# Performance work log

Hardware: AMD Instinct MI355X
Metric: run time of the kernel (lower is better)

## Reference

```python
import jax, jax.numpy as jnp
import numpy as np

# dims
N, E, Z, C, NB = 8192, 131072, 10, 128, 8
R_MAX, P_CUT, AVG_NEIGH = 5.0, 5, 16.0
SH_DIM, N_L, N_LAYERS, MLP_H = 16, 4, 2, 16
# which l each of the 16 sh components belongs to
L_OF_M = jnp.array([0, 1, 1, 1, 2, 2, 2, 2, 2, 3, 3, 3, 3, 3, 3, 3])


def spherical_harmonics(u):
    """Real spherical harmonics up to l=3, e3nn 'component' normalization. u: [E,3] unit vectors."""
    x, y, z = u[:, 0], u[:, 1], u[:, 2]
    x2, y2, z2 = x * x, y * y, z * z
    s3, s5, s15 = np.sqrt(3.0), np.sqrt(5.0), np.sqrt(15.0)
    a33, a32, a31, a30 = 0.25 * np.sqrt(70.0), np.sqrt(105.0), 0.25 * np.sqrt(42.0), 0.5 * np.sqrt(7.0)
    Y = [jnp.ones_like(x),
         s3 * x, s3 * y, s3 * z,
         s15 * x * y, s15 * y * z, 0.5 * s5 * (3 * z2 - 1.0), s15 * x * z, 0.5 * s15 * (x2 - y2),
         a33 * y * (3 * x2 - y2), a32 * x * y * z, a31 * y * (5 * z2 - 1.0),
         a30 * z * (5 * z2 - 3.0), a31 * x * (5 * z2 - 1.0), 0.5 * a32 * z * (x2 - y2),
         a33 * x * (x2 - 3 * y2)]
    return jnp.stack(Y, axis=-1)  # [E,16]


def radial_embedding(r):
    """Bessel radial basis with smooth polynomial cutoff (p=5). r: [E] edge lengths."""
    x = r / R_MAX
    p = float(P_CUT)
    cut = (1.0 - 0.5 * (p + 1.0) * (p + 2.0) * x ** P_CUT
           + p * (p + 2.0) * x ** (P_CUT + 1) - 0.5 * p * (p + 1.0) * x ** (P_CUT + 2))
    cut = jnp.where(x < 1.0, cut, 0.0)
    n = jnp.arange(1, NB + 1, dtype=r.dtype)
    bessel = np.sqrt(2.0 / R_MAX) * jnp.sin(n[None, :] * jnp.pi * x[:, None]) / r[:, None]
    return bessel * cut[:, None]  # [E,8]


def _forward(positions, node_attrs, shifts, W_embed, W_up, R_w1, R_w2, R_w3,
             W_out, w_sc, w_prod, W_plin, w_ro0, ro_w1, ro_w2, edge_index):
    sender, receiver = edge_index[0], edge_index[1]
    vec = positions[receiver] - positions[sender] + shifts          # [E,3]
    lengths = jnp.linalg.norm(vec, axis=-1) + 1e-9                  # [E]
    sh = spherical_harmonics(vec / lengths[:, None])                # [E,16]
    edge_feats = radial_embedding(lengths)                          # [E,8]

    # node embedding: scalars into l=0 slot of [N,C,16]
    scalars = node_attrs @ W_embed                                  # [N,C]
    feats = jnp.zeros((N, C, SH_DIM), scalars.dtype).at[:, :, 0].set(scalars)

    outputs = []
    for L in range(N_LAYERS):
        # linear up (channel mixing, per irrep component)
        h = jnp.einsum('ncm,cd->ndm', feats, W_up[L])               # [N,C,16]
        # radial MLP -> per-edge, per-channel, per-l tensor-product weights
        r = jax.nn.silu(edge_feats @ R_w1[L])
        r = jax.nn.silu(r @ R_w2[L])
        w = (r @ R_w3[L]).reshape(E, C, N_L)                        # [E,C,4]
        w_m = jnp.take(w, L_OF_M, axis=2)                           # [E,C,16]
        # channel-wise tensor product: scalar node feat x SH, scatter to receiver
        msg = h[sender, :, 0][:, :, None] * w_m * sh[:, None, :]    # [E,C,16]
        agg = jax.ops.segment_sum(msg, receiver, num_segments=N) / AVG_NEIGH
        m = jnp.einsum('ncm,cd->ndm', agg, W_out[L])                # [N,C,16]
        # element-dependent skip connection
        sc = h * (node_attrs @ w_sc[L])[:, :, None]
        # product basis (correlation 3): element-weighted powers of scalar part
        s = m[:, :, 0]                                              # [N,C]
        coeff = jnp.einsum('nz,zck->nck', node_attrs, w_prod[L])    # [N,C,3]
        powers = jnp.stack([jnp.ones_like(s), s, s * s], axis=-1)   # [N,C,3]
        scale = jnp.sum(coeff * powers, axis=-1)                    # [N,C]
        feats = jnp.einsum('ncm,cd->ndm', m * scale[:, :, None], W_plin[L]) + sc
        if L == 0:
            outputs.append(feats[:, :, 0] @ w_ro0)                  # linear readout [N]
        else:
            outputs.append(jax.nn.silu(feats[:, :, 0] @ ro_w1) @ ro_w2)  # nonlinear readout [N]
    return outputs[0] + outputs[1]


def setup_inputs() -> dict:
    key = jax.random.key(0)
    ks = jax.random.split(key, 16)
    positions = jax.random.normal(ks[0], (N, 3), jnp.float32) * 1.5
    elems = jax.random.randint(ks[1], (N,), 0, Z)
    node_attrs = jax.nn.one_hot(elems, Z, dtype=jnp.float32)
    edge_index = jax.random.randint(ks[2], (2, E), 0, N)
    shifts = jnp.zeros((E, 3), jnp.float32)
    g = lambda k, sh, fan: jax.random.normal(k, sh, jnp.float32) / np.sqrt(fan)
    return {
        'positions': positions, 'node_attrs': node_attrs, 'shifts': shifts,
        'W_embed': g(ks[3], (Z, C), Z),
        'W_up': g(ks[4], (N_LAYERS, C, C), C),
        'R_w1': g(ks[5], (N_LAYERS, NB, 64), NB),
        'R_w2': g(ks[6], (N_LAYERS, 64, 64), 64),
        'R_w3': g(ks[7], (N_LAYERS, 64, C * N_L), 64),
        'W_out': g(ks[8], (N_LAYERS, C, C), C),
        'w_sc': g(ks[9], (N_LAYERS, Z, C), 1),
        'w_prod': g(ks[10], (N_LAYERS, Z, C, 3), 1) * 0.1,
        'W_plin': g(ks[11], (N_LAYERS, C, C), C),
        'w_ro0': g(ks[12], (C,), C),
        'ro_w1': g(ks[13], (C, MLP_H), C),
        'ro_w2': g(ks[14], (MLP_H,), MLP_H),
        'edge_index': edge_index,
    }


def reference(positions, node_attrs, shifts, W_embed, W_up, R_w1, R_w2, R_w3,
              W_out, w_sc, w_prod, W_plin, w_ro0, ro_w1, ro_w2, edge_index):
    return _forward(positions, node_attrs, shifts, W_embed, W_up, R_w1, R_w2, R_w3,
                    W_out, w_sc, w_prod, W_plin, w_ro0, ro_w1, ro_w2, edge_index)
```

## Files before the change

kernel.cpp:

```cpp
#include <hip/hip_runtime.h>
#include <math.h>

constexpr int kN = 8192;
constexpr int kE = 131072;
constexpr int NPB = 16;

typedef short bf16x8 __attribute__((ext_vector_type(8)));
typedef float f32x4 __attribute__((ext_vector_type(4)));
typedef unsigned short ushort_t;
typedef unsigned int uint_t;

__device__ __forceinline__ float silu_f(float x) { return x / (1.f + __expf(-x)); }

__device__ __forceinline__ ushort_t f2b(float f) {
  uint_t x = __float_as_uint(f);
  uint_t r = (x + 0x7fffu + ((x >> 16) & 1u)) >> 16;
  return (ushort_t)r;
}
__device__ __forceinline__ float b2f(ushort_t u) {
  return __uint_as_float(((uint_t)u) << 16);
}

__global__ __launch_bounds__(256) void zero_ints_kernel(int* __restrict__ a, int* __restrict__ b) {
  int i = blockIdx.x * 256 + threadIdx.x;
  if (i < kN) { a[i] = 0; b[i] = 0; }
}

__global__ __launch_bounds__(256) void elem_kernel(const float* __restrict__ attrs, int* __restrict__ elem) {
  int n = blockIdx.x * 256 + threadIdx.x;
  if (n >= kN) return;
  const float* a = attrs + (size_t)n * 10;
  int best = 0; float bv = a[0];
  #pragma unroll
  for (int z = 1; z < 10; ++z) { float v = a[z]; if (v > bv) { bv = v; best = z; } }
  elem[n] = best;
}

__global__ __launch_bounds__(256) void init_feats_kernel(const float* __restrict__ W_embed,
                                                         const int* __restrict__ elem,
                                                         ushort_t* __restrict__ F) {
  int i = blockIdx.x * 256 + threadIdx.x;
  int n = i >> 7, c = i & 127;
  F[(size_t)n * 2048 + c] = f2b(W_embed[(size_t)elem[n] * 128 + c]);
}

__global__ __launch_bounds__(256) void count_kernel(const int* __restrict__ ei, int* __restrict__ counts) {
  int e = blockIdx.x * 256 + threadIdx.x;
  if (e < kE) atomicAdd(&counts[ei[kE + e]], 1);
}

__global__ __launch_bounds__(1024) void scan_kernel(const int* __restrict__ counts, int* __restrict__ offs) {
  __shared__ int tmp[1024];
  int t = threadIdx.x;
  int loc[8]; int s = 0;
  #pragma unroll
  for (int i = 0; i < 8; ++i) { loc[i] = s; s += counts[t*8 + i]; }
  tmp[t] = s;
  __syncthreads();
  for (int d = 1; d < 1024; d <<= 1) {
    int v = (t >= d) ? tmp[t - d] : 0;
    __syncthreads();
    tmp[t] += v;
    __syncthreads();
  }
  int pre = (t == 0) ? 0 : tmp[t - 1];
  #pragma unroll
  for (int i = 0; i < 8; ++i) offs[t*8 + i] = pre + loc[i];
  if (t == 1023) offs[kN] = tmp[1023];
}

__global__ __launch_bounds__(256) void fill_kernel(const int* __restrict__ ei, const int* __restrict__ offs,
                                                   int* __restrict__ cursor, int* __restrict__ eids,
                                                   int* __restrict__ sends) {
  int e = blockIdx.x * 256 + threadIdx.x;
  if (e >= kE) return;
  int s = ei[e];
  int r = ei[kE + e];
  int pos = atomicAdd(&cursor[r], 1);
  eids[offs[r] + pos] = e;
  sends[offs[r] + pos] = s;
}

__global__ __launch_bounds__(256) void geom_kernel(const float* __restrict__ pos,
                                                   const float* __restrict__ shifts,
                                                   const int* __restrict__ ei,
                                                   const int* __restrict__ eids,
                                                   const int* __restrict__ sends,
                                                   float* __restrict__ sh,
                                                   float* __restrict__ rb) {
  int slot = blockIdx.x * 256 + threadIdx.x;
  if (slot >= kE) return;
  int e = eids[slot];
  int s = sends[slot];
  int r = ei[kE + e];
  float vx = pos[r*3+0] - pos[s*3+0] + shifts[(size_t)e*3+0];
  float vy = pos[r*3+1] - pos[s*3+1] + shifts[(size_t)e*3+1];
  float vz = pos[r*3+2] - pos[s*3+2] + shifts[(size_t)e*3+2];
  float len = sqrtf(vx*vx + vy*vy + vz*vz) + 1e-9f;
  float inv = 1.f / len;
  float x = vx*inv, y = vy*inv, z = vz*inv;
  float x2 = x*x, y2 = y*y, z2 = z*z;
  const float s3  = 1.7320508075688772f;
  const float s5  = 2.2360679774997896f;
  const float s15 = 3.8729833462074170f;
  const float a33 = 2.0916500663351889f;
  const float a32 = 10.246950765959598f;
  const float a31 = 1.6201851746019651f;
  const float a30 = 1.3228756555322954f;
  float4* shp = (float4*)(sh + (size_t)slot * 16);
  shp[0] = make_float4(1.f, s3*x, s3*y, s3*z);
  shp[1] = make_float4(s15*x*y, s15*y*z, 0.5f*s5*(3.f*z2 - 1.f), s15*x*z);
  shp[2] = make_float4(0.5f*s15*(x2 - y2), a33*y*(3.f*x2 - y2), a32*x*y*z, a31*y*(5.f*z2 - 1.f));
  shp[3] = make_float4(a30*z*(5.f*z2 - 3.f), a31*x*(5.f*z2 - 1.f), 0.5f*a32*z*(x2 - y2), a33*x*(x2 - 3.f*y2));
  float xr = len * 0.2f;
  float cut = 0.f;
  if (xr < 1.f) {
    float x5 = xr*xr*xr*xr*xr;
    cut = 1.f - 21.f*x5 + 35.f*x5*xr - 15.f*x5*xr*xr;
  }
  float pref = 0.63245553203367587f * cut * inv;
  const float PI = 3.14159265358979323846f;
  float theta = PI * xr;
  float sn, cs;
  __sincosf(theta, &sn, &cs);
  float twoc = 2.f * cs;
  float b[8];
  float s_prev = 0.f, s_cur = sn;
  b[0] = pref * s_cur;
  #pragma unroll
  for (int k = 1; k < 8; ++k) {
    float s_next = twoc * s_cur - s_prev;
    s_prev = s_cur; s_cur = s_next;
    b[k] = pref * s_cur;
  }
  float4* rbp = (float4*)(rb + (size_t)slot * 8);
  rbp[0] = make_float4(b[0], b[1], b[2], b[3]);
  rbp[1] = make_float4(b[4], b[5], b[6], b[7]);
}

__global__ __launch_bounds__(256) void radial_kernel(const float* __restrict__ rb,
                                                     const float* __restrict__ W1,
                                                     const float* __restrict__ W2,
                                                     ushort_t* __restrict__ r2) {
  __shared__ float rbs[128][8];
  __shared__ float W1s[8*64];
  __shared__ ushort_t B2s[64][72];
  __shared__ ushort_t r1s[128][72];
  const int tid = threadIdx.x;
  const size_t ebase = (size_t)blockIdx.x * 128;
  {
    int r = tid >> 1, q = tid & 1;
    *(float4*)&rbs[r][q*4] = *(const float4*)&rb[(ebase + r)*8 + q*4];
  }
  for (int i = tid; i < 512; i += 256) W1s[i] = W1[i];
  for (int i = tid; i < 4096; i += 256) {
    int k = i >> 6, col = i & 63;
    B2s[col][k] = f2b(W2[i]);
  }
  __syncthreads();
  {
    int col = tid & 63;
    int r0 = (tid >> 6) * 32;
    #pragma unroll 4
    for (int rr = 0; rr < 32; ++rr) {
      int row = r0 + rr;
      float v = 0.f;
      #pragma unroll
      for (int i = 0; i < 8; ++i) v = fmaf(rbs[row][i], W1s[i*64 + col], v);
      r1s[row][col] = f2b(silu_f(v));
    }
  }
  __syncthreads();
  const int lane = tid & 63, wv = tid >> 6;
  const int wr = wv * 32;
  const int fr = lane & 15, kg = (lane >> 4) * 8;
  f32x4 acc[2][4] = {};
  #pragma unroll
  for (int ks = 0; ks < 2; ++ks) {
    const int k0 = ks*32 + kg;
    bf16x8 af[2], bfr[4];
    #pragma unroll
    for (int i = 0; i < 2; ++i) af[i] = *(const bf16x8*)&r1s[wr + i*16 + fr][k0];
    #pragma unroll
    for (int j = 0; j < 4; ++j) bfr[j] = *(const bf16x8*)&B2s[j*16 + fr][k0];
    #pragma unroll
    for (int i = 0; i < 2; ++i)
      #pragma unroll
      for (int j = 0; j < 4; ++j)
        acc[i][j] = __builtin_amdgcn_mfma_f32_16x16x32_bf16(af[i], bfr[j], acc[i][j], 0, 0, 0);
  }
  __syncthreads();
  const int dcol = lane & 15, drow4 = (lane >> 4) * 4;
  #pragma unroll
  for (int i = 0; i < 2; ++i)
    #pragma unroll
    for (int j = 0; j < 4; ++j)
      #pragma unroll
      for (int r = 0; r < 4; ++r) {
        int row = wr + i*16 + drow4 + r;
        int col = j*16 + dcol;
        r1s[row][col] = f2b(silu_f(acc[i][j][r]));
      }
  __syncthreads();
  for (int idx = tid * 8; idx < 128*64; idx += 256*8) {
    int r = idx >> 6, k = idx & 63;
    *(int4*)&r2[(ebase + r)*64 + k] = *(const int4*)&r1s[r][k];
  }
}

__global__ __launch_bounds__(256) void transpose_w_kernel(const float* __restrict__ W, ushort_t* __restrict__ WT) {
  int i = blockIdx.x * 256 + threadIdx.x;
  int d = i >> 7, c = i & 127;
  WT[i] = f2b(W[c*128 + d]);
}

__global__ __launch_bounds__(256) void transpose_r3_kernel(const float* __restrict__ R3, ushort_t* __restrict__ R3T) {
  int i = blockIdx.x * 256 + threadIdx.x;
  int t = i >> 6, j = i & 63;
  int c = t & 127, l = t >> 7;
  R3T[i] = f2b(R3[j*512 + c*4 + l]);
}

template<bool SCALED, bool EPI, bool L0>
__global__ __launch_bounds__(256) void mgemm_kernel(
    const ushort_t* __restrict__ A, size_t aStride,
    const ushort_t* __restrict__ BT,
    ushort_t* __restrict__ O, size_t oStride,
    const float* __restrict__ scaleBuf,
    const ushort_t* __restrict__ Hbuf,
    const float* __restrict__ wscL,
    const int* __restrict__ elem)
{
  __shared__ ushort_t As[128][136];
  __shared__ ushort_t Bs[128][136];
  const int tid = threadIdx.x;
  const size_t rowbase = (size_t)blockIdx.x * 128;

  for (int idx = tid * 8; idx < 128 * 128; idx += 256 * 8) {
    int r = idx >> 7, k = idx & 127;
    *(int4*)&Bs[r][k] = *(const int4*)&BT[(size_t)r * 128 + k];
  }
  for (int idx = tid * 8; idx < 128 * 128; idx += 256 * 8) {
    int r = idx >> 7, k = idx & 127;
    size_t grow = rowbase + r;
    const ushort_t* ap = A + grow * aStride + k;
    if (SCALED) {
      const float* sp = scaleBuf + (grow >> 4) * 128 + k;
      uint_t u[4];
      #pragma unroll
      for (int q = 0; q < 4; ++q) {
        ushort_t lo = f2b(b2f(ap[2*q])   * sp[2*q]);
        ushort_t hi = f2b(b2f(ap[2*q+1]) * sp[2*q+1]);
        u[q] = (uint_t)lo | ((uint_t)hi << 16);
      }
      *(int4*)&As[r][k] = make_int4((int)u[0], (int)u[1], (int)u[2], (int)u[3]);
    } else {
      *(int4*)&As[r][k] = *(const int4*)ap;
    }
  }
  __syncthreads();

  const int lane = tid & 63, wv = tid >> 6;
  const int wr = (wv >> 1) * 64, wc = (wv & 1) * 64;
  const int fr = lane & 15;
  const int kg = (lane >> 4) * 8;
  f32x4 acc[4][4] = {};
  #pragma unroll
  for (int ks = 0; ks < 4; ++ks) {
    const int k0 = ks * 32 + kg;
    bf16x8 af[4], bfr[4];
    #pragma unroll
    for (int i = 0; i < 4; ++i) af[i]  = *(const bf16x8*)&As[wr + i*16 + fr][k0];
    #pragma unroll
    for (int j = 0; j < 4; ++j) bfr[j] = *(const bf16x8*)&Bs[wc + j*16 + fr][k0];
    #pragma unroll
    for (int i = 0; i < 4; ++i)
      #pragma unroll
      for (int j = 0; j < 4; ++j)
        acc[i][j] = __builtin_amdgcn_mfma_f32_16x16x32_bf16(af[i], bfr[j], acc[i][j], 0, 0, 0);
  }

  const int dcol = lane & 15, drow4 = (lane >> 4) * 4;
  #pragma unroll
  for (int i = 0; i < 4; ++i) {
    #pragma unroll
    for (int j = 0; j < 4; ++j) {
      int col = wc + j*16 + dcol;
      #pragma unroll
      for (int r = 0; r < 4; ++r) {
        int row = wr + i*16 + drow4 + r;
        size_t grow = rowbase + row;
        float v = acc[i][j][r];
        if (EPI) {
          if (!L0 || ((grow & 15) == 0)) {
            int ee = elem[grow >> 4];
            v += b2f(Hbuf[grow * 128 + col]) * wscL[(size_t)ee * 128 + col];
          }
        }
        O[grow * oStride + col] = f2b(v);
      }
    }
  }
}

__global__ __launch_bounds__(512, 1) void gather_kernel(
    const int* __restrict__ offs, const int* __restrict__ sends,
    const ushort_t* __restrict__ r2csr,
    const float* __restrict__ shcsr,
    const ushort_t* __restrict__ R3T,
    const ushort_t* __restrict__ H,
    ushort_t* __restrict__ AGG)
{
  __shared__ ushort_t R3Ts[512][68];
  __shared__ ushort_t r2s[2][32][68];
  __shared__ ushort_t h0s[2][32][132];
  __shared__ float    shs[2][32][16];
  const int tid = threadIdx.x;
  const int lane = tid & 63, wid = tid >> 6;
  const int l = wid >> 1, cb = (wid & 1) * 64;
  const int mb = l * l, mc = 2 * l + 1;
  const int fr = lane & 15, kg = (lane >> 4) * 8;
  const int n0 = blockIdx.x * NPB;
  const int hslot = tid >> 4, hseg = tid & 15;
  const int rslot = tid >> 3, rseg = tid & 7;
  const int xs = tid - 256, sslot = xs >> 2, sseg = xs & 3;

  for (int idx = tid; idx < 4096; idx += 512) {
    int tr = idx >> 3, seg = idx & 7;
    *(int4*)&R3Ts[tr][seg * 8] = *(const int4*)&R3T[(size_t)tr * 64 + seg * 8];
  }
  {
    int a0 = offs[n0], a1 = offs[n0 + 1];
    int4 h0v = make_int4(0,0,0,0), r2v = make_int4(0,0,0,0);
    float4 shv = make_float4(0.f,0.f,0.f,0.f);
    if (a0 + hslot < a1) h0v = *(const int4*)&H[(size_t)sends[a0 + hslot] * 2048 + hseg * 8];
    if (tid < 256 && a0 + rslot < a1) r2v = *(const int4*)&r2csr[(size_t)(a0 + rslot) * 64 + rseg * 8];
    if (tid >= 256 && tid < 384 && a0 + sslot < a1) shv = *(const float4*)&shcsr[(size_t)(a0 + sslot) * 16 + sseg * 4];
    *(int4*)&h0s[0][hslot][hseg * 8] = h0v;
    if (tid < 256) *(int4*)&r2s[0][rslot][rseg * 8] = r2v;
    else if (tid < 384) *(float4*)&shs[0][sslot][sseg * 4] = shv;
  }
  __syncthreads();

  int p = 0;
  for (int nn = n0; nn < n0 + NPB; ++nn) {
    const int e0n = offs[nn], e1n = offs[nn + 1];
    int4 h0n = make_int4(0,0,0,0), r2n = make_int4(0,0,0,0);
    float4 shn = make_float4(0.f,0.f,0.f,0.f);
    if (nn + 1 < n0 + NPB) {
      int a0 = offs[nn + 1], a1 = offs[nn + 2];
      if (a0 + hslot < a1) h0n = *(const int4*)&H[(size_t)sends[a0 + hslot] * 2048 + hseg * 8];
      if (tid < 256 && a0 + rslot < a1) r2n = *(const int4*)&r2csr[(size_t)(a0 + rslot) * 64 + rseg * 8];
      if (tid >= 256 && tid < 384 && a0 + sslot < a1) shn = *(const float4*)&shcsr[(size_t)(a0 + sslot) * 16 + sseg * 4];
    }

    float agg[7][4] = {};
    auto compute = [&](int pb) {
      f32x4 acc[2][4] = {};
      #pragma unroll
      for (int ks = 0; ks < 2; ++ks) {
        bf16x8 af[2], bfr[4];
        #pragma unroll
        for (int i = 0; i < 2; ++i) af[i] = *(const bf16x8*)&r2s[pb][i*16 + fr][ks*32 + kg];
        #pragma unroll
        for (int j = 0; j < 4; ++j) bfr[j] = *(const bf16x8*)&R3Ts[wid*64 + j*16 + fr][ks*32 + kg];
        #pragma unroll
        for (int i = 0; i < 2; ++i)
          #pragma unroll
          for (int j = 0; j < 4; ++j)
            acc[i][j] = __builtin_amdgcn_mfma_f32_16x16x32_bf16(af[i], bfr[j], acc[i][j], 0, 0, 0);
      }
      #pragma unroll
      for (int i = 0; i < 2; ++i)
        #pragma unroll
        for (int r = 0; r < 4; ++r) {
          int slot = i*16 + ((lane >> 4) << 2) + r;
          float shr[7];
          #pragma unroll
          for (int mi = 0; mi < 7; ++mi) shr[mi] = shs[pb][slot][mb + mi];
          #pragma unroll
          for (int j = 0; j < 4; ++j) {
            float wh = acc[i][j][r] * b2f(h0s[pb][slot][cb + j*16 + fr]);
            #pragma unroll
            for (int mi = 0; mi < 7; ++mi)
              if (mi < mc) agg[mi][j] = fmaf(wh, shr[mi], agg[mi][j]);
          }
        }
    };
    compute(p);
    for (int base = e0n + 32; base < e1n; base += 32) {
      __syncthreads();
      int4 h0x = make_int4(0,0,0,0), r2x = make_int4(0,0,0,0);
      float4 shx = make_float4(0.f,0.f,0.f,0.f);
      if (base + hslot < e1n) h0x = *(const int4*)&H[(size_t)sends[base + hslot] * 2048 + hseg * 8];
      if (tid < 256 && base + rslot < e1n) r2x = *(const int4*)&r2csr[(size_t)(base + rslot) * 64 + rseg * 8];
      if (tid >= 256 && tid < 384 && base + sslot < e1n) shx = *(const float4*)&shcsr[(size_t)(base + sslot) * 16 + sseg * 4];
      *(int4*)&h0s[p][hslot][hseg * 8] = h0x;
      if (tid < 256) *(int4*)&r2s[p][rslot][rseg * 8] = r2x;
      else if (tid < 384) *(float4*)&shs[p][sslot][sseg * 4] = shx;
      __syncthreads();
      compute(p);
    }
    #pragma unroll
    for (int mi = 0; mi < 7; ++mi) {
      if (mi < mc) {
        #pragma unroll
        for (int j = 0; j < 4; ++j) {
          float v = agg[mi][j];
          v += __shfl_xor(v, 16, 64);
          v += __shfl_xor(v, 32, 64);
          if (lane < 16)
            AGG[(size_t)nn * 2048 + (mb + mi) * 128 + cb + j * 16 + lane] = f2b(v * 0.0625f);
        }
      }
    }
    *(int4*)&h0s[p ^ 1][hslot][hseg * 8] = h0n;
    if (tid < 256) *(int4*)&r2s[p ^ 1][rslot][rseg * 8] = r2n;
    else if (tid < 384) *(float4*)&shs[p ^ 1][sslot][sseg * 4] = shn;
    __syncthreads();
    p ^= 1;
  }
}

__global__ __launch_bounds__(256) void scale_kernel(const ushort_t* __restrict__ M,
                                                    const int* __restrict__ elem,
                                                    const float* __restrict__ wprodL,
                                                    float* __restrict__ scale) {
  int i = blockIdx.x * 256 + threadIdx.x;
  int n = i >> 7, c = i & 127;
  float s = b2f(M[(size_t)n * 2048 + c]);
  const float* co = wprodL + ((size_t)elem[n] * 128 + c) * 3;
  scale[i] = co[0] + s * (co[1] + s * co[2]);
}

__global__ __launch_bounds__(64) void readout_kernel(const ushort_t* __restrict__ F,
                                                     const float* __restrict__ ro0,
                                                     const float* __restrict__ ro1,
                                                     const float* __restrict__ ro2,
                                                     float* __restrict__ out, int layer) {
  int n = blockIdx.x; int t = threadIdx.x;
  const ushort_t* fr = F + (size_t)n * 2048;
  float f0 = b2f(fr[t]), f1 = b2f(fr[t + 64]);
  if (layer == 0) {
    float v = f0 * ro0[t] + f1 * ro0[t + 64];
    #pragma unroll
    for (int m = 32; m > 0; m >>= 1) v += __shfl_xor(v, m, 64);
    if (t == 0) out[n] = v;
  } else {
    float acc = 0.f;
    for (int h = 0; h < 16; ++h) {
      float p = f0 * ro1[t*16 + h] + f1 * ro1[(t + 64)*16 + h];
      #pragma unroll
      for (int m = 32; m > 0; m >>= 1) p += __shfl_xor(p, m, 64);
      acc = fmaf(silu_f(p), ro2[h], acc);
    }
    if (t == 0) out[n] += acc;
  }
}

extern "C" void kernel_launch(void* const* d_in, const int* in_sizes, int n_in,
                              void* d_out, int out_size, void* d_ws, size_t ws_size,
                              hipStream_t stream) {
  (void)in_sizes; (void)n_in; (void)out_size;
  const float* positions = (const float*)d_in[0];
  const float* node_attrs= (const float*)d_in[1];
  const float* shifts    = (const float*)d_in[2];
  const float* W_embed   = (const float*)d_in[3];
  const float* W_up      = (const float*)d_in[4];
  const float* R_w1      = (const float*)d_in[5];
  const float* R_w2      = (const float*)d_in[6];
  const float* R_w3      = (const float*)d_in[7];
  const float* W_out     = (const float*)d_in[8];
  const float* w_sc      = (const float*)d_in[9];
  const float* w_prod    = (const float*)d_in[10];
  const float* W_plin    = (const float*)d_in[11];
  const float* w_ro0     = (const float*)d_in[12];
  const float* ro_w1     = (const float*)d_in[13];
  const float* ro_w2     = (const float*)d_in[14];
  const int*   ei        = (const int*)d_in[15];
  float* out = (float*)d_out;

  char* ws_ptr = (char*)d_ws;
  size_t off = 0;
  auto alloc = [&](size_t nbytes) -> void* {
    void* p = ws_ptr + off;
    off += (nbytes + 255) & ~(size_t)255;
    return p;
  };
  const size_t PB = (size_t)kN * 16 * 128 * sizeof(ushort_t);
  ushort_t* P0    = (ushort_t*)alloc(PB);
  ushort_t* P1    = (ushort_t*)alloc(PB);
  ushort_t* P2    = (ushort_t*)alloc(PB);
  float* shcsr    = (float*)alloc((size_t)kE * 16 * 4);
  float* rbcsr    = (float*)alloc((size_t)kE * 8 * 4);
  ushort_t* r2csr = (ushort_t*)alloc((size_t)kE * 64 * 2);
  float* scaleb   = (float*)alloc((size_t)kN * 128 * 4);
  ushort_t* R3T0  = (ushort_t*)alloc(512 * 64 * 2);
  ushort_t* R3T1  = (ushort_t*)alloc(512 * 64 * 2);
  ushort_t* WTu0  = (ushort_t*)alloc(128 * 128 * 2);
  ushort_t* WTu1  = (ushort_t*)alloc(128 * 128 * 2);
  ushort_t* WTo0  = (ushort_t*)alloc(128 * 128 * 2);
  ushort_t* WTo1  = (ushort_t*)alloc(128 * 128 * 2);
  ushort_t* WTp0  = (ushort_t*)alloc(128 * 128 * 2);
  ushort_t* WTp1  = (ushort_t*)alloc(128 * 128 * 2);
  int* elemb  = (int*)alloc(kN * 4);
  int* counts = (int*)alloc(kN * 4);
  int* cursor = (int*)alloc(kN * 4);
  int* offsb  = (int*)alloc((kN + 1) * 4);
  int* eidsb  = (int*)alloc((size_t)kE * 4);
  int* sendsb = (int*)alloc((size_t)kE * 4);
  if (off > ws_size) return;

  zero_ints_kernel<<<kN/256, 256, 0, stream>>>(counts, cursor);
  elem_kernel<<<kN/256, 256, 0, stream>>>(node_attrs, elemb);
  init_feats_kernel<<<(kN*128)/256, 256, 0, stream>>>(W_embed, elemb, P0);
  count_kernel<<<kE/256, 256, 0, stream>>>(ei, counts);
  scan_kernel<<<1, 1024, 0, stream>>>(counts, offsb);
  fill_kernel<<<kE/256, 256, 0, stream>>>(ei, offsb, cursor, eidsb, sendsb);
  geom_kernel<<<kE/256, 256, 0, stream>>>(positions, shifts, ei, eidsb, sendsb, shcsr, rbcsr);
  transpose_w_kernel<<<64, 256, 0, stream>>>(W_up, WTu0);
  transpose_w_kernel<<<64, 256, 0, stream>>>(W_up + 16384, WTu1);
  transpose_w_kernel<<<64, 256, 0, stream>>>(W_out, WTo0);
  transpose_w_kernel<<<64, 256, 0, stream>>>(W_out + 16384, WTo1);
  transpose_w_kernel<<<64, 256, 0, stream>>>(W_plin, WTp0);
  transpose_w_kernel<<<64, 256, 0, stream>>>(W_plin + 16384, WTp1);
  transpose_r3_kernel<<<128, 256, 0, stream>>>(R_w3, R3T0);
  transpose_r3_kernel<<<128, 256, 0, stream>>>(R_w3 + 32768, R3T1);

  radial_kernel<<<kE/128, 256, 0, stream>>>(rbcsr, R_w1, R_w2, r2csr);
  mgemm_kernel<false,false,false><<<kN/128, 256, 0, stream>>>(
      P0, 2048, WTu0, P1, 2048, nullptr, nullptr, nullptr, nullptr);
  gather_kernel<<<kN/NPB, 512, 0, stream>>>(offsb, sendsb, r2csr, shcsr, R3T0, P1, P2);
  mgemm_kernel<false,false,false><<<(kN*16)/128, 256, 0, stream>>>(
      P2, 128, WTo0, P0, 128, nullptr, nullptr, nullptr, nullptr);
  scale_kernel<<<(kN*128)/256, 256, 0, stream>>>(P0, elemb, w_prod, scaleb);
  mgemm_kernel<true,true,true><<<(kN*16)/128, 256, 0, stream>>>(
      P0, 128, WTp0, P2, 128, scaleb, P1, w_sc, elemb);
  readout_kernel<<<kN, 64, 0, stream>>>(P2, w_ro0, ro_w1, ro_w2, out, 0);

  radial_kernel<<<kE/128, 256, 0, stream>>>(rbcsr, R_w1 + 512, R_w2 + 4096, r2csr);
  mgemm_kernel<false,false,false><<<(kN*16)/128, 256, 0, stream>>>(
      P2, 128, WTu1, P1, 128, nullptr, nullptr, nullptr, nullptr);
  gather_kernel<<<kN/NPB, 512, 0, stream>>>(offsb, sendsb, r2csr, shcsr, R3T1, P1, P0);
  mgemm_kernel<false,false,false><<<(kN*16)/128, 256, 0, stream>>>(
      P0, 128, WTo1, P2, 128, nullptr, nullptr, nullptr, nullptr);
  scale_kernel<<<(kN*128)/256, 256, 0, stream>>>(P2, elemb, w_prod + 3840, scaleb);
  mgemm_kernel<true,true,false><<<(kN*16)/128, 256, 0, stream>>>(
      P2, 128, WTp1, P0, 128, scaleb, P1, w_sc + 1280, elemb);
  readout_kernel<<<kN, 64, 0, stream>>>(P0, w_ro0, ro_w1, ro_w2, out, 1);
}
```

Before: 546.3 us.

## Split gather kernel channel halves across grid y with smaller blocks

```diff
diff --git a/kernel.cpp b/kernel.cpp
--- a/kernel.cpp
+++ b/kernel.cpp
@@ -303,7 +303,7 @@
   }
 }
 
-__global__ __launch_bounds__(512, 1) void gather_kernel(
+__global__ __launch_bounds__(256, 2) void gather_kernel(
     const int* __restrict__ offs, const int* __restrict__ sends,
     const ushort_t* __restrict__ r2csr,
     const float* __restrict__ shcsr,
@@ -311,34 +311,39 @@
     const ushort_t* __restrict__ H,
     ushort_t* __restrict__ AGG)
 {
-  __shared__ ushort_t R3Ts[512][68];
+  __shared__ ushort_t R3Ts[256][68];
   __shared__ ushort_t r2s[2][32][68];
-  __shared__ ushort_t h0s[2][32][132];
-  __shared__ float    shs[2][32][16];
+  __shared__ ushort_t h0s[2][32][68];
+  __shared__ float    shs[2][32][17];
   const int tid = threadIdx.x;
-  const int lane = tid & 63, wid = tid >> 6;
-  const int l = wid >> 1, cb = (wid & 1) * 64;
+  const int lane = tid & 63;
+  const int l = tid >> 6;
+  const int cbb = blockIdx.y * 64;
   const int mb = l * l, mc = 2 * l + 1;
-  const int fr = lane & 15, kg = (lane >> 4) * 8;
+  const int fr = lane & 15, g = lane >> 4, kg = g * 8;
   const int n0 = blockIdx.x * NPB;
-  const int hslot = tid >> 4, hseg = tid & 15;
-  const int rslot = tid >> 3, rseg = tid & 7;
-  const int xs = tid - 256, sslot = xs >> 2, sseg = xs & 3;
-
-  for (int idx = tid; idx < 4096; idx += 512) {
-    int tr = idx >> 3, seg = idx & 7;
-    *(int4*)&R3Ts[tr][seg * 8] = *(const int4*)&R3T[(size_t)tr * 64 + seg * 8];
+  const int hslot = tid >> 3, hseg = tid & 7;
+  const int s0i = tid, s1i = 256 + tid;
+
+  for (int idx = tid; idx < 2048; idx += 256) {
+    int lt = idx >> 3, seg = idx & 7;
+    int gt = (lt >> 6) * 128 + cbb + (lt & 63);
+    *(int4*)&R3Ts[lt][seg * 8] = *(const int4*)&R3T[(size_t)gt * 64 + seg * 8];
   }
   {
     int a0 = offs[n0], a1 = offs[n0 + 1];
     int4 h0v = make_int4(0,0,0,0), r2v = make_int4(0,0,0,0);
-    float4 shv = make_float4(0.f,0.f,0.f,0.f);
-    if (a0 + hslot < a1) h0v = *(const int4*)&H[(size_t)sends[a0 + hslot] * 2048 + hseg * 8];
-    if (tid < 256 && a0 + rslot < a1) r2v = *(const int4*)&r2csr[(size_t)(a0 + rslot) * 64 + rseg * 8];
-    if (tid >= 256 && tid < 384 && a0 + sslot < a1) shv = *(const float4*)&shcsr[(size_t)(a0 + sslot) * 16 + sseg * 4];
+    float sv0 = 0.f, sv1 = 0.f;
+    if (a0 + hslot < a1) {
+      h0v = *(const int4*)&H[(size_t)sends[a0 + hslot] * 2048 + cbb + hseg * 8];
+      r2v = *(const int4*)&r2csr[(size_t)(a0 + hslot) * 64 + hseg * 8];
+    }
+    if (a0 + (s0i >> 4) < a1) sv0 = shcsr[(size_t)(a0 + (s0i >> 4)) * 16 + (s0i & 15)];
+    if (a0 + (s1i >> 4) < a1) sv1 = shcsr[(size_t)(a0 + (s1i >> 4)) * 16 + (s1i & 15)];
     *(int4*)&h0s[0][hslot][hseg * 8] = h0v;
-    if (tid < 256) *(int4*)&r2s[0][rslot][rseg * 8] = r2v;
-    else if (tid < 384) *(float4*)&shs[0][sslot][sseg * 4] = shv;
+    *(int4*)&r2s[0][hslot][hseg * 8] = r2v;
+    shs[0][s0i >> 4][s0i & 15] = sv0;
+    shs[0][s1i >> 4][s1i & 15] = sv1;
   }
   __syncthreads();
 
@@ -346,12 +351,15 @@
   for (int nn = n0; nn < n0 + NPB; ++nn) {
     const int e0n = offs[nn], e1n = offs[nn + 1];
     int4 h0n = make_int4(0,0,0,0), r2n = make_int4(0,0,0,0);
-    float4 shn = make_float4(0.f,0.f,0.f,0.f);
+    float sn0 = 0.f, sn1 = 0.f;
     if (nn + 1 < n0 + NPB) {
       int a0 = offs[nn + 1], a1 = offs[nn + 2];
-      if (a0 + hslot < a1) h0n = *(const int4*)&H[(size_t)sends[a0 + hslot] * 2048 + hseg * 8];
-      if (tid < 256 && a0 + rslot < a1) r2n = *(const int4*)&r2csr[(size_t)(a0 + rslot) * 64 + rseg * 8];
-      if (tid >= 256 && tid < 384 && a0 + sslot < a1) shn = *(const float4*)&shcsr[(size_t)(a0 + sslot) * 16 + sseg * 4];
+      if (a0 + hslot < a1) {
+        h0n = *(const int4*)&H[(size_t)sends[a0 + hslot] * 2048 + cbb + hseg * 8];
+        r2n = *(const int4*)&r2csr[(size_t)(a0 + hslot) * 64 + hseg * 8];
+      }
+      if (a0 + (s0i >> 4) < a1) sn0 = shcsr[(size_t)(a0 + (s0i >> 4)) * 16 + (s0i & 15)];
+      if (a0 + (s1i >> 4) < a1) sn1 = shcsr[(size_t)(a0 + (s1i >> 4)) * 16 + (s1i & 15)];
     }
 
     float agg[7][4] = {};
@@ -363,7 +371,7 @@
         #pragma unroll
         for (int i = 0; i < 2; ++i) af[i] = *(const bf16x8*)&r2s[pb][i*16 + fr][ks*32 + kg];
         #pragma unroll
-        for (int j = 0; j < 4; ++j) bfr[j] = *(const bf16x8*)&R3Ts[wid*64 + j*16 + fr][ks*32 + kg];
+        for (int j = 0; j < 4; ++j) bfr[j] = *(const bf16x8*)&R3Ts[l*64 + j*16 + fr][ks*32 + kg];
         #pragma unroll
         for (int i = 0; i < 2; ++i)
           #pragma unroll
@@ -374,13 +382,13 @@
       for (int i = 0; i < 2; ++i)
         #pragma unroll
         for (int r = 0; r < 4; ++r) {
-          int slot = i*16 + ((lane >> 4) << 2) + r;
+          int slot = i*16 + g*4 + r;
           float shr[7];
           #pragma unroll
           for (int mi = 0; mi < 7; ++mi) shr[mi] = shs[pb][slot][mb + mi];
           #pragma unroll
           for (int j = 0; j < 4; ++j) {
-            float wh = acc[i][j][r] * b2f(h0s[pb][slot][cb + j*16 + fr]);
+            float wh = acc[i][j][r] * b2f(h0s[pb][slot][j*16 + fr]);
             #pragma unroll
             for (int mi = 0; mi < 7; ++mi)
               if (mi < mc) agg[mi][j] = fmaf(wh, shr[mi], agg[mi][j]);
@@ -391,13 +399,17 @@
     for (int base = e0n + 32; base < e1n; base += 32) {
       __syncthreads();
       int4 h0x = make_int4(0,0,0,0), r2x = make_int4(0,0,0,0);
-      float4 shx = make_float4(0.f,0.f,0.f,0.f);
-      if (base + hslot < e1n) h0x = *(const int4*)&H[(size_t)sends[base + hslot] * 2048 + hseg * 8];
-      if (tid < 256 && base + rslot < e1n) r2x = *(const int4*)&r2csr[(size_t)(base + rslot) * 64 + rseg * 8];
-      if (tid >= 256 && tid < 384 && base + sslot < e1n) shx = *(const float4*)&shcsr[(size_t)(base + sslot) * 16 + sseg * 4];
+      float sx0 = 0.f, sx1 = 0.f;
+      if (base + hslot < e1n) {
+        h0x = *(const int4*)&H[(size_t)sends[base + hslot] * 2048 + cbb + hseg * 8];
+        r2x = *(const int4*)&r2csr[(size_t)(base + hslot) * 64 + hseg * 8];
+      }
+      if (base + (s0i >> 4) < e1n) sx0 = shcsr[(size_t)(base + (s0i >> 4)) * 16 + (s0i & 15)];
+      if (base + (s1i >> 4) < e1n) sx1 = shcsr[(size_t)(base + (s1i >> 4)) * 16 + (s1i & 15)];
       *(int4*)&h0s[p][hslot][hseg * 8] = h0x;
-      if (tid < 256) *(int4*)&r2s[p][rslot][rseg * 8] = r2x;
-      else if (tid < 384) *(float4*)&shs[p][sslot][sseg * 4] = shx;
+      *(int4*)&r2s[p][hslot][hseg * 8] = r2x;
+      shs[p][s0i >> 4][s0i & 15] = sx0;
+      shs[p][s1i >> 4][s1i & 15] = sx1;
       __syncthreads();
       compute(p);
     }
@@ -410,13 +422,14 @@
           v += __shfl_xor(v, 16, 64);
           v += __shfl_xor(v, 32, 64);
           if (lane < 16)
-            AGG[(size_t)nn * 2048 + (mb + mi) * 128 + cb + j * 16 + lane] = f2b(v * 0.0625f);
+            AGG[(size_t)nn * 2048 + (mb + mi) * 128 + cbb + j * 16 + lane] = f2b(v * 0.0625f);
         }
       }
     }
     *(int4*)&h0s[p ^ 1][hslot][hseg * 8] = h0n;
-    if (tid < 256) *(int4*)&r2s[p ^ 1][rslot][rseg * 8] = r2n;
-    else if (tid < 384) *(float4*)&shs[p ^ 1][sslot][sseg * 4] = shn;
+    *(int4*)&r2s[p ^ 1][hslot][hseg * 8] = r2n;
+    shs[p ^ 1][s0i >> 4][s0i & 15] = sn0;
+    shs[p ^ 1][s1i >> 4][s1i & 15] = sn1;
     __syncthreads();
     p ^= 1;
   }
@@ -530,7 +543,7 @@
   radial_kernel<<<kE/128, 256, 0, stream>>>(rbcsr, R_w1, R_w2, r2csr);
   mgemm_kernel<false,false,false><<<kN/128, 256, 0, stream>>>(
       P0, 2048, WTu0, P1, 2048, nullptr, nullptr, nullptr, nullptr);
-  gather_kernel<<<kN/NPB, 512, 0, stream>>>(offsb, sendsb, r2csr, shcsr, R3T0, P1, P2);
+  gather_kernel<<<dim3(kN/NPB, 2), 256, 0, stream>>>(offsb, sendsb, r2csr, shcsr, R3T0, P1, P2);
   mgemm_kernel<false,false,false><<<(kN*16)/128, 256, 0, stream>>>(
       P2, 128, WTo0, P0, 128, nullptr, nullptr, nullptr, nullptr);
   scale_kernel<<<(kN*128)/256, 256, 0, stream>>>(P0, elemb, w_prod, scaleb);
@@ -541,7 +554,7 @@
   radial_kernel<<<kE/128, 256, 0, stream>>>(rbcsr, R_w1 + 512, R_w2 + 4096, r2csr);
   mgemm_kernel<false,false,false><<<(kN*16)/128, 256, 0, stream>>>(
       P2, 128, WTu1, P1, 128, nullptr, nullptr, nullptr, nullptr);
-  gather_kernel<<<kN/NPB, 512, 0, stream>>>(offsb, sendsb, r2csr, shcsr, R3T1, P1, P0);
+  gather_kernel<<<dim3(kN/NPB, 2), 256, 0, stream>>>(offsb, sendsb, r2csr, shcsr, R3T1, P1, P0);
   mgemm_kernel<false,false,false><<<(kN*16)/128, 256, 0, stream>>>(
       P0, 128, WTo1, P2, 128, nullptr, nullptr, nullptr, nullptr);
   scale_kernel<<<(kN*128)/256, 256, 0, stream>>>(P2, elemb, w_prod + 3840, scaleb);
```

After: 508.5 us. 6.9% less time.
